# Kernel tuning notes

Measured on AMD Instinct MI355X. Metric: run time of the kernel, lower is better.

Reference implementation:

```python
import jax, jax.numpy as jnp
import numpy as np
import math

N_HEADS = 12
HEAD_SIZE = 64
D_MODEL = 768
N_BASIS = 256
LENGTH = 1024
BATCH = 8
INV_SQRT_2PI = 1.0 / math.sqrt(2.0 * math.pi)


def _phi(t):
    # standard normal pdf
    return INV_SQRT_2PI * jnp.exp(-0.5 * t * t)


def _make_basis():
    # get_gaussian_basis_functions: meshgrid(linspace(0,1,N/2), sigmas).flatten()
    sigmas = np.array([0.01, 0.05], dtype=np.float32)
    mus = np.linspace(0.0, 1.0, N_BASIS // 2, dtype=np.float32)
    mu_b = np.repeat(mus, 2)          # [N]
    sigma_b = np.tile(sigmas, N_BASIS // 2)  # [N]
    return jnp.asarray(mu_b), jnp.asarray(sigma_b)


def _make_G(mu_b, sigma_b, klen, ridge=1.0):
    # compute_G: positions (i+1)/l, F[j,i] = psi_j(pos_i), G = F^T (F F^T + I)^{-1}
    pos = jnp.arange(1, klen + 1, dtype=jnp.float32) / klen
    F = _phi((pos[None, :] - mu_b[:, None]) / sigma_b[:, None]) / sigma_b[:, None]  # [N, klen]
    A = F @ F.T + ridge * jnp.eye(N_BASIS, dtype=jnp.float32)
    return F.T @ jnp.linalg.inv(A)  # [klen, N]


def setup_inputs() -> dict:
    key = jax.random.key(0)
    ks = jax.random.split(key, 8)
    sc = 1.0 / math.sqrt(D_MODEL)
    x = jax.random.normal(ks[0], (LENGTH, BATCH, D_MODEL), jnp.float32)
    q = jax.random.normal(ks[1], (LENGTH, BATCH, D_MODEL), jnp.float32)
    Wq = jax.random.normal(ks[2], (D_MODEL, D_MODEL), jnp.float32) * sc
    Wk = jax.random.normal(ks[3], (D_MODEL, D_MODEL), jnp.float32) * sc
    Wv = jax.random.normal(ks[4], (D_MODEL, D_MODEL), jnp.float32) * sc
    Wo = jax.random.normal(ks[5], (D_MODEL, D_MODEL), jnp.float32) * sc
    w_mu = jax.random.normal(ks[6], (N_BASIS,), jnp.float32) * (1.0 / math.sqrt(N_BASIS))
    w_sigma = jax.random.normal(ks[7], (N_BASIS,), jnp.float32) * (1.0 / math.sqrt(N_BASIS))
    mu_b, sigma_b = _make_basis()
    G = _make_G(mu_b, sigma_b, LENGTH)
    return {"x": x, "q": q, "Wq": Wq, "Wk": Wk, "Wv": Wv, "Wo": Wo,
            "w_mu": w_mu, "w_sigma": w_sigma, "mu_b": mu_b, "sigma_b": sigma_b, "G": G}


def reference(x, q, Wq, Wk, Wv, Wo, w_mu, w_sigma, mu_b, sigma_b, G):
    klen, B, d = x.shape
    qlen = q.shape[0]
    H, dh = N_HEADS, HEAD_SIZE
    # value_function: compress memory onto basis coefficients, B_mat: [B, N, d]
    Bmat = jnp.einsum('lbd,ln->bnd', x, G)
    keys = (Bmat @ Wk.T).reshape(B, N_BASIS, H, dh).transpose(0, 2, 1, 3)    # [B,H,N,dh]
    values = (Bmat @ Wv.T).reshape(B, N_BASIS, H, dh).transpose(0, 2, 1, 3)  # [B,H,N,dh]
    query = (q.transpose(1, 0, 2) @ Wq.T).reshape(B, qlen, H, dh).transpose(0, 2, 1, 3)
    scores = jnp.einsum('bhqe,bhne->bhqn', query, keys) / math.sqrt(dh)      # [B,H,q,N]
    # attention distribution parameters (theta -> (mu, sigma_sq) exactly)
    mu = jax.nn.sigmoid(scores @ w_mu)          # [B,H,q]
    sigma_sq = jax.nn.softplus(scores @ w_sigma)  # [B,H,q]
    # ContinuousSoftmax forward: E_{N(mu,sigma_sq)}[psi_j]
    #   = N(mu; mu_b_j, sigma_b_j^2 + sigma_sq)   (product-of-Gaussians integral)
    s = jnp.sqrt(sigma_b[None, None, None, :] ** 2 + sigma_sq[..., None])
    r = _phi((mu[..., None] - mu_b[None, None, None, :]) / s) / s            # [B,H,q,N]
    context = jnp.einsum('bhqn,bhnd->bhqd', r, values)                       # [B,H,q,dh]
    context = context.transpose(0, 2, 1, 3).reshape(B, qlen, H * dh)
    return context @ Wo.T  # [B, qlen, d_model]
```

## Files before the change

### kernel.cpp

```cpp
#include <hip/hip_runtime.h>
#include <hip/hip_bf16.h>
#include <math.h>

#define NHEADS 12
#define HEAD   64
#define DM     768
#define NB     256
#define SLEN   1024
#define NBATCH 8

typedef __bf16 bf16x8 __attribute__((ext_vector_type(8)));
typedef float  f32x4  __attribute__((ext_vector_type(4)));

__device__ __forceinline__ float gload(const void* p, long i, int bf) {
  return bf ? __bfloat162float(((const __hip_bfloat16*)p)[i])
            : ((const float*)p)[i];
}

__global__ void detect_dtype(const void* x, int* flag) {
  __shared__ float red[256];
  int t = threadIdx.x;
  const __hip_bfloat16* p = (const __hip_bfloat16*)x;
  float a = fabsf(__bfloat162float(p[t * 2]));
  float b = fabsf(__bfloat162float(p[t * 2 + 1]));
  float m = fmaxf(a, b);
  red[t] = m;
  __syncthreads();
  for (int s = 128; s > 0; s >>= 1) {
    if (t < s) red[t] = fmaxf(red[t], red[t + s]);
    __syncthreads();
  }
  if (t == 0) flag[0] = (red[0] < 1e4f) ? 1 : 0;
}

__global__ void convertk(const void* __restrict__ src, float* __restrict__ dst,
                         int n, const int* __restrict__ flagp) {
  int bf = flagp[0];
  int i = blockIdx.x * 256 + threadIdx.x;
  if (i < n) dst[i] = gload(src, i, bf);
}

__global__ __launch_bounds__(256) void zerok(float* __restrict__ p, long n) {
  long i = ((long)blockIdx.x * 256 + threadIdx.x) * 4;
  if (i < n) {
    f32x4 z = {0.f, 0.f, 0.f, 0.f};
    *(f32x4*)(p + i) = z;
  }
}

__global__ __launch_bounds__(256) void split4(
    const void* __restrict__ src, __hip_bfloat16* __restrict__ dh,
    __hip_bfloat16* __restrict__ dl, int n, const int* __restrict__ flagp,
    int use_flag) {
  int bf = use_flag ? flagp[0] : 0;
  int i0 = (blockIdx.x * 256 + threadIdx.x) * 4;
  if (i0 >= n) return;
#pragma unroll
  for (int j = 0; j < 4; j++) {
    float f = gload(src, i0 + j, bf);
    __hip_bfloat16 h = __float2bfloat16(f);
    dh[i0 + j] = h;
    dl[i0 + j] = __float2bfloat16(f - __bfloat162float(h));
  }
}

__global__ __launch_bounds__(256) void tsplit(
    const void* __restrict__ src, __hip_bfloat16* __restrict__ dh,
    __hip_bfloat16* __restrict__ dl, int R, int C,
    const int* __restrict__ flagp) {
  int bf = flagp[0];
  __shared__ float t[64][65];
  int r0 = blockIdx.y * 64, c0 = blockIdx.x * 64;
  int cl = threadIdx.x & 63, rl = threadIdx.x >> 6;
#pragma unroll
  for (int i = 0; i < 16; i++) {
    int rr = rl + i * 4;
    t[rr][cl] = gload(src, (long)(r0 + rr) * C + c0 + cl, bf);
  }
  __syncthreads();
#pragma unroll
  for (int i = 0; i < 16; i++) {
    int cc = rl + i * 4;
    float f = t[cl][cc];
    __hip_bfloat16 h = __float2bfloat16(f);
    long o = (long)(c0 + cc) * R + r0 + cl;
    dh[o] = h;
    dl[o] = __float2bfloat16(f - __bfloat162float(h));
  }
}

__global__ __launch_bounds__(256) void vtsplit(
    const float* __restrict__ src, __hip_bfloat16* __restrict__ dh,
    __hip_bfloat16* __restrict__ dl) {
  __shared__ float tle[64][65];
  const int z = blockIdx.y;
  const int r0 = blockIdx.x * 64;
  const float* s = src + (long)z * 16384;
  int cl = threadIdx.x & 63, rl4 = threadIdx.x >> 6;
#pragma unroll
  for (int i = 0; i < 16; i++) {
    int rr = rl4 + i * 4;
    tle[rr][cl] = s[(r0 + rr) * 64 + cl];
  }
  __syncthreads();
#pragma unroll
  for (int i = 0; i < 16; i++) {
    int cc = rl4 + i * 4;
    float f = tle[cl][cc];
    __hip_bfloat16 h = __float2bfloat16(f);
    long o = (long)z * 16384 + (long)cc * 256 + r0 + cl;
    dh[o] = h;
    dl[o] = __float2bfloat16(f - __bfloat162float(h));
  }
}

__device__ __forceinline__ void stage_tile(
    const __hip_bfloat16* __restrict__ src, int ld, __hip_bfloat16* lds, int t) {
  int row = t >> 2;
  int col = (t & 3) * 8;
  int wavebase = (t >> 6) * 1024;
#pragma unroll
  for (int i = 0; i < 2; i++) {
    const __hip_bfloat16* gp = src + (long)(i * 64 + row) * ld + col;
    __builtin_amdgcn_global_load_lds(
        (const __attribute__((address_space(1))) void*)gp,
        (__attribute__((address_space(3))) void*)((char*)lds + i * 4096 + wavebase),
        16, 0, 0);
  }
}

__global__ __launch_bounds__(256) void mfma_nt_lds(
    const __hip_bfloat16* __restrict__ Ah_g, const __hip_bfloat16* __restrict__ Al_g,
    const __hip_bfloat16* __restrict__ Wh_g, const __hip_bfloat16* __restrict__ Wl_g,
    void* __restrict__ Cout, int K, int lda, int ldb, long a_batch, long c_batch,
    int om, int oh, const int* __restrict__ flagp, int use_flag, int pmask_bf,
    int ksplit) {
  int flag = flagp[0];
  int bf = use_flag ? flag : 0;
  __shared__ __hip_bfloat16 As0[4096], As1[4096];
  __shared__ __hip_bfloat16 Bs0[4096], Bs1[4096];

  const int gx = gridDim.x, gy = gridDim.y;
  const int nwg = gx * gy * gridDim.z;
  const int lin = (blockIdx.z * gy + blockIdx.y) * gx + blockIdx.x;
  const int swz = (lin & 7) * (nwg >> 3) + (lin >> 3);
  const int bx = swz % gx;
  const int rem = swz / gx;
  const int by = rem % gy;
  const int bzf = rem / gy;
  const int bz = bzf / ksplit;
  const int kc = bzf - bz * ksplit;
  const int Ks = K / ksplit;
  const int kbeg = kc * Ks, kend = kbeg + Ks;

  const int m0 = by * 128, n0 = bx * 128;
  const int t = threadIdx.x;
  const int lane = t & 63;
  const int r = lane & 15, g = lane >> 4;
  const int wave = t >> 6;
  const int wm = (wave >> 1) * 64, wn = (wave & 1) * 64;

  const __hip_bfloat16* Abh = Ah_g + (long)bz * a_batch;
  const __hip_bfloat16* Abl = Al_g + (long)bz * a_batch;

  f32x4 zero4 = {0.f, 0.f, 0.f, 0.f};
  f32x4 acc[4][4];
#pragma unroll
  for (int fi = 0; fi < 4; fi++)
#pragma unroll
    for (int fj = 0; fj < 4; fj++) acc[fi][fj] = zero4;

  for (int pass = 0; pass < 3; pass++) {
    if (flag && !((pmask_bf >> pass) & 1)) continue;
    const __hip_bfloat16* Arow = ((pass < 2) ? Abh : Abl) + (long)m0 * lda;
    const __hip_bfloat16* Brow = ((pass == 1) ? Wl_g : Wh_g) + (long)n0 * ldb;
    stage_tile(Arow + kbeg, lda, As0, t);
    stage_tile(Brow + kbeg, ldb, Bs0, t);
    __syncthreads();
    int cur = 0;
    for (int k0 = kbeg; k0 < kend; k0 += 32) {
      const __hip_bfloat16* Asc = cur ? As1 : As0;
      const __hip_bfloat16* Bsc = cur ? Bs1 : Bs0;
      bf16x8 af[4], bw[4];
#pragma unroll
      for (int fi = 0; fi < 4; fi++)
        af[fi] = *(const bf16x8*)(Asc + (wm + fi * 16 + r) * 32 + g * 8);
#pragma unroll
      for (int fj = 0; fj < 4; fj++)
        bw[fj] = *(const bf16x8*)(Bsc + (wn + fj * 16 + r) * 32 + g * 8);
      if (k0 + 32 < kend) {
        stage_tile(Arow + k0 + 32, lda, cur ? As0 : As1, t);
        stage_tile(Brow + k0 + 32, ldb, cur ? Bs0 : Bs1, t);
      }
#pragma unroll
      for (int fi = 0; fi < 4; fi++)
#pragma unroll
        for (int fj = 0; fj < 4; fj++)
          acc[fi][fj] = __builtin_amdgcn_mfma_f32_16x16x32_bf16(
              af[fi], bw[fj], acc[fi][fj], 0, 0, 0);
      __syncthreads();
      cur ^= 1;
    }
  }

  if (ksplit > 1) {
    float* Cf = (float*)Cout;
#pragma unroll
    for (int fi = 0; fi < 4; fi++)
#pragma unroll
      for (int fj = 0; fj < 4; fj++)
#pragma unroll
        for (int v = 0; v < 4; v++) {
          int m = m0 + wm + fi * 16 + g * 4 + v;
          int n = n0 + wn + fj * 16 + r;
          long off = (long)bz * c_batch + (long)m * om + (long)(n >> 6) * oh + (n & 63);
          atomicAdd(Cf + off, acc[fi][fj][v]);
        }
  } else {
#pragma unroll
    for (int fi = 0; fi < 4; fi++)
#pragma unroll
      for (int fj = 0; fj < 4; fj++)
#pragma unroll
        for (int v = 0; v < 4; v++) {
          int m = m0 + wm + fi * 16 + g * 4 + v;
          int n = n0 + wn + fj * 16 + r;
          long off = (long)bz * c_batch + (long)m * om + (long)(n >> 6) * oh + (n & 63);
          float val = acc[fi][fj][v];
          if (bf) ((__hip_bfloat16*)Cout)[off] = __float2bfloat16(val);
          else    ((float*)Cout)[off] = val;
        }
  }
}

__global__ __launch_bounds__(256) void bvec(
    const float* __restrict__ Bmat, const float* __restrict__ wmuf,
    const float* __restrict__ wsigf, float* __restrict__ bmu,
    float* __restrict__ bsig) {
  int t = blockIdx.x * 256 + threadIdx.x;
  int w = t / 6144, r = t % 6144;
  const float* wv = w ? wsigf : wmuf;
  float acc = 0.f;
  for (int n = 0; n < NB; n++) acc += wv[n] * Bmat[(long)n * 6144 + r];
  (w ? bsig : bmu)[r] = acc;
}

__global__ __launch_bounds__(256) void kvec(
    const float* __restrict__ Wkf, const float* __restrict__ bmu,
    const float* __restrict__ bsig, float* __restrict__ kmu,
    float* __restrict__ ksig) {
  int t = blockIdx.x * 256 + threadIdx.x;
  int w = t / 6144, r = t % 6144;
  int b = r / 768, c = r % 768;
  const float* bv = (w ? bsig : bmu) + b * 768;
  const float* wk = Wkf + (long)c * 768;
  float acc = 0.f;
  for (int d = 0; d < 768; d++) acc += bv[d] * wk[d];
  (w ? ksig : kmu)[r] = acc;
}

__global__ __launch_bounds__(256) void wqvec(
    const float* __restrict__ Wqf, const float* __restrict__ kmu,
    const float* __restrict__ ksig, float* __restrict__ wqm,
    float* __restrict__ wqs) {
  int t = blockIdx.x * 256 + threadIdx.x;
  int w = t / 73728, r = t % 73728;
  int b = r / 9216, h = (r % 9216) / 768, d = r % 768;
  const float* kv = (w ? ksig : kmu) + b * 768 + h * 64;
  float acc = 0.f;
  for (int dh = 0; dh < 64; dh++)
    acc += Wqf[(long)(h * 64 + dh) * 768 + d] * kv[dh];
  (w ? wqs : wqm)[r] = acc;
}

__global__ __launch_bounds__(256) void amu_kernel(
    const void* __restrict__ q, const float* __restrict__ wqm,
    const float* __restrict__ wqs, float* __restrict__ amu,
    const int* __restrict__ flagp) {
  int bf = flagp[0];
  int lane = threadIdx.x & 63;
  int wave = threadIdx.x >> 6;
  int qrow = blockIdx.x * 4 + wave;
  int b = blockIdx.y;
  float qv[12];
  long base = ((long)qrow * 8 + b) * 768 + lane;
#pragma unroll
  for (int j = 0; j < 12; j++) qv[j] = gload(q, base + 64 * j, bf);
  for (int hh = 0; hh < 24; hh++) {
    const float* vec = (hh < 12) ? (wqm + ((long)b * 12 + hh) * 768)
                                 : (wqs + ((long)b * 12 + hh - 12) * 768);
    float p = 0.f;
#pragma unroll
    for (int j = 0; j < 12; j++) p += qv[j] * vec[lane + 64 * j];
#pragma unroll
    for (int m = 32; m >= 1; m >>= 1) p += __shfl_xor(p, m);
    if (lane == 0) amu[((long)b * 24 + hh) * 1024 + qrow] = p;
  }
}

__global__ __launch_bounds__(256) void attn_mfma(
    const __hip_bfloat16* __restrict__ Vth, const __hip_bfloat16* __restrict__ Vtl,
    const float* __restrict__ amu, const float* __restrict__ mubf,
    const float* __restrict__ sigbf, __hip_bfloat16* __restrict__ Ch,
    __hip_bfloat16* __restrict__ Cl) {
  const int qch = blockIdx.x, h = blockIdx.y, b = blockIdx.z;
  const int t = threadIdx.x;
  const int lane = t & 63, wave = t >> 6;
  const int r = lane & 15, g = lane >> 4;
  const int wq = wave * 32;
  __shared__ float s_mub[NB], s_sb2[NB];
  {
    float sb = sigbf[t];
    s_mub[t] = mubf[t];
    s_sb2[t] = sb * sb;
  }
  __syncthreads();

  float mu_[2], sig_[2];
#pragma unroll
  for (int fi = 0; fi < 2; fi++) {
    int q = qch * 128 + wq + fi * 16 + r;
    float araw = amu[((long)b * 24 + h) * 1024 + q] * 0.125f;
    float sraw = amu[((long)b * 24 + 12 + h) * 1024 + q] * 0.125f;
    mu_[fi] = 1.f / (1.f + expf(-araw));
    sig_[fi] = fmaxf(sraw, 0.f) + log1pf(expf(-fabsf(sraw)));
  }

  const __hip_bfloat16* vhb = Vth + ((long)b * 12 + h) * 16384;
  const __hip_bfloat16* vlb = Vtl + ((long)b * 12 + h) * 16384;

  f32x4 zero4 = {0.f, 0.f, 0.f, 0.f};
  f32x4 acc[2][4];
#pragma unroll
  for (int fi = 0; fi < 2; fi++)
#pragma unroll
    for (int fj = 0; fj < 4; fj++) acc[fi][fj] = zero4;

  for (int ks = 0; ks < 8; ks++) {
    bf16x8 rh[2], rl[2];
#pragma unroll
    for (int fi = 0; fi < 2; fi++) {
      float mu = mu_[fi], sg = sig_[fi];
#pragma unroll
      for (int j = 0; j < 8; j++) {
        int n = ks * 32 + g * 8 + j;
        float inv_s = rsqrtf(s_sb2[n] + sg);
        float tt = (mu - s_mub[n]) * inv_s;
        float rv = 0.3989422804014327f * inv_s *
                   exp2f(-0.7213475204444817f * tt * tt);
        __bf16 hi = (__bf16)rv;
        rh[fi][j] = hi;
        rl[fi][j] = (__bf16)(rv - (float)hi);
      }
    }
#pragma unroll
    for (int fj = 0; fj < 4; fj++) {
      long vo = (long)(fj * 16 + r) * 256 + ks * 32 + g * 8;
      bf16x8 vh = *(const bf16x8*)(vhb + vo);
      bf16x8 vl = *(const bf16x8*)(vlb + vo);
#pragma unroll
      for (int fi = 0; fi < 2; fi++) {
        acc[fi][fj] = __builtin_amdgcn_mfma_f32_16x16x32_bf16(
            rh[fi], vh, acc[fi][fj], 0, 0, 0);
        acc[fi][fj] = __builtin_amdgcn_mfma_f32_16x16x32_bf16(
            rl[fi], vh, acc[fi][fj], 0, 0, 0);
        acc[fi][fj] = __builtin_amdgcn_mfma_f32_16x16x32_bf16(
            rh[fi], vl, acc[fi][fj], 0, 0, 0);
      }
    }
  }

#pragma unroll
  for (int fi = 0; fi < 2; fi++)
#pragma unroll
    for (int fj = 0; fj < 4; fj++)
#pragma unroll
      for (int v = 0; v < 4; v++) {
        int q = qch * 128 + wq + fi * 16 + g * 4 + v;
        int d = fj * 16 + r;
        long off = ((long)(b * SLEN + q)) * DM + h * HEAD + d;
        float f = acc[fi][fj][v];
        __hip_bfloat16 hh = __float2bfloat16(f);
        Ch[off] = hh;
        Cl[off] = __float2bfloat16(f - __bfloat162float(hh));
      }
}

extern "C" void kernel_launch(void* const* d_in, const int* in_sizes, int n_in,
                              void* d_out, int out_size, void* d_ws, size_t ws_size,
                              hipStream_t stream) {
  const void* x    = d_in[0];
  const void* q    = d_in[1];
  const void* Wq   = d_in[2];
  const void* Wk   = d_in[3];
  const void* Wv   = d_in[4];
  const void* Wo   = d_in[5];
  const void* wmu  = d_in[6];
  const void* wsig = d_in[7];
  const void* mub  = d_in[8];
  const void* sigb = d_in[9];
  const void* G    = d_in[10];

  int* flagp = (int*)d_ws;
  float* base = (float*)d_ws + 16;
  float* Wqf   = base;
  float* Wkf   = Wqf + 589824;
  float* wmuf  = Wkf + 589824;
  float* wsigf = wmuf + 256;
  float* mubf  = wsigf + 256;
  float* sigbf = mubf + 256;
  float* Bmat  = sigbf + 256;
  float* values= Bmat + 1572864;
  float* bmu   = values + 1572864;
  float* bsig  = bmu + 6144;
  float* kmu   = bsig + 6144;
  float* ksig  = kmu + 6144;
  float* wqm   = ksig + 6144;
  float* wqs   = wqm + 73728;
  float* amu   = wqs + 73728;
  __hip_bfloat16* Wvh = (__hip_bfloat16*)(amu + 196608);
  __hip_bfloat16* Wvl = Wvh + 589824;
  __hip_bfloat16* Woh = Wvl + 589824;
  __hip_bfloat16* Wol = Woh + 589824;
  __hip_bfloat16* Gth = Wol + 589824;
  __hip_bfloat16* Gtl = Gth + 262144;
  __hip_bfloat16* Bh  = Gtl + 262144;
  __hip_bfloat16* Bl  = Bh + 1572864;
  __hip_bfloat16* XCh = Bl + 1572864;
  __hip_bfloat16* XCl = XCh + 6291456;
  __hip_bfloat16* Vth = XCl + 6291456;
  __hip_bfloat16* Vtl = Vth + 1572864;

  detect_dtype<<<1, 256, 0, stream>>>(x, flagp);

  convertk<<<2304, 256, 0, stream>>>(Wq, Wqf, 589824, flagp);
  convertk<<<2304, 256, 0, stream>>>(Wk, Wkf, 589824, flagp);
  convertk<<<1, 256, 0, stream>>>(wmu, wmuf, 256, flagp);
  convertk<<<1, 256, 0, stream>>>(wsig, wsigf, 256, flagp);
  convertk<<<1, 256, 0, stream>>>(mub, mubf, 256, flagp);
  convertk<<<1, 256, 0, stream>>>(sigb, sigbf, 256, flagp);

  tsplit<<<dim3(4, 16), 256, 0, stream>>>(G, Gth, Gtl, 1024, 256, flagp);
  tsplit<<<dim3(96, 16), 256, 0, stream>>>(x, XCh, XCl, 1024, 6144, flagp);
  split4<<<576, 256, 0, stream>>>(Wv, Wvh, Wvl, 589824, flagp, 1);
  split4<<<576, 256, 0, stream>>>(Wo, Woh, Wol, 589824, flagp, 1);

  zerok<<<1536, 256, 0, stream>>>(Bmat, 1572864);
  mfma_nt_lds<<<dim3(48, 2, 8), 256, 0, stream>>>(
      Gth, Gtl, XCh, XCl, Bmat, 1024, 1024, 1024,
      0, 0, 6144, 64, flagp, 0,
      1, 8);

  split4<<<1536, 256, 0, stream>>>(Bmat, Bh, Bl, 1572864, flagp, 0);

  zerok<<<1536, 256, 0, stream>>>(values, 1572864);
  mfma_nt_lds<<<dim3(6, 2, 64), 256, 0, stream>>>(
      Bh, Bl, Wvh, Wvl, values, 768, 6144, 768,
      768, 196608, 64, 16384, flagp, 0,
      5, 8);

  vtsplit<<<dim3(4, 96), 256, 0, stream>>>(values, Vth, Vtl);

  bvec<<<48, 256, 0, stream>>>(Bmat, wmuf, wsigf, bmu, bsig);
  kvec<<<48, 256, 0, stream>>>(Wkf, bmu, bsig, kmu, ksig);
  wqvec<<<576, 256, 0, stream>>>(Wqf, kmu, ksig, wqm, wqs);
  amu_kernel<<<dim3(256, 8), 256, 0, stream>>>(q, wqm, wqs, amu, flagp);

  attn_mfma<<<dim3(8, 12, 8), 256, 0, stream>>>(
      Vth, Vtl, amu, mubf, sigbf, XCh, XCl);

  mfma_nt_lds<<<dim3(6, 64, 1), 256, 0, stream>>>(
      XCh, XCl, Woh, Wol, d_out, 768, 768, 768,
      0, 0, 768, 64, flagp, 1,
      5, 1);
}
```

Baseline: 423.1 us.

## Fuse prep launches, replace atomic split-K with slabs, fuse vector chain

Merges the separate convert, transpose-split and split kernels into one multi-role prep launch, cutting the number of launches. The split-K GEMMs now use 4 splits instead of 8 and write partial results to separate slabs instead of using atomicAdd into zeroed buffers. Follow-up kernels sum the slabs and fuse that sum with the bf16 hi/lo split, so the zeroing kernels go away. The bvec, kvec and wqvec kernels are fused into a single 16-block chain kernel. The trade-offs are that this chain kernel has far less parallelism, that the slabs take more memory traffic, and that one slab buffer is aliased onto the XC buffer.

```diff
diff --git a/kernel.cpp b/kernel.cpp
--- a/kernel.cpp
+++ b/kernel.cpp
@@ -33,84 +33,79 @@
   if (t == 0) flag[0] = (red[0] < 1e4f) ? 1 : 0;
 }
 
-__global__ void convertk(const void* __restrict__ src, float* __restrict__ dst,
-                         int n, const int* __restrict__ flagp) {
-  int bf = flagp[0];
-  int i = blockIdx.x * 256 + threadIdx.x;
-  if (i < n) dst[i] = gload(src, i, bf);
-}
-
-__global__ __launch_bounds__(256) void zerok(float* __restrict__ p, long n) {
-  long i = ((long)blockIdx.x * 256 + threadIdx.x) * 4;
-  if (i < n) {
-    f32x4 z = {0.f, 0.f, 0.f, 0.f};
-    *(f32x4*)(p + i) = z;
-  }
-}
-
-__global__ __launch_bounds__(256) void split4(
-    const void* __restrict__ src, __hip_bfloat16* __restrict__ dh,
-    __hip_bfloat16* __restrict__ dl, int n, const int* __restrict__ flagp,
-    int use_flag) {
-  int bf = use_flag ? flagp[0] : 0;
-  int i0 = (blockIdx.x * 256 + threadIdx.x) * 4;
-  if (i0 >= n) return;
-#pragma unroll
-  for (int j = 0; j < 4; j++) {
-    float f = gload(src, i0 + j, bf);
-    __hip_bfloat16 h = __float2bfloat16(f);
-    dh[i0 + j] = h;
-    dl[i0 + j] = __float2bfloat16(f - __bfloat162float(h));
-  }
-}
-
-__global__ __launch_bounds__(256) void tsplit(
-    const void* __restrict__ src, __hip_bfloat16* __restrict__ dh,
-    __hip_bfloat16* __restrict__ dl, int R, int C,
+__global__ __launch_bounds__(256) void prep(
+    const void* __restrict__ Wq, const void* __restrict__ Wk,
+    const void* __restrict__ wmu, const void* __restrict__ wsig,
+    const void* __restrict__ mub, const void* __restrict__ sigb,
+    const void* __restrict__ G, const void* __restrict__ x,
+    const void* __restrict__ Wv, const void* __restrict__ Wo,
+    float* __restrict__ Wqf, float* __restrict__ Wkf,
+    float* __restrict__ wmuf, float* __restrict__ wsigf,
+    float* __restrict__ mubf, float* __restrict__ sigbf,
+    __hip_bfloat16* __restrict__ Gth, __hip_bfloat16* __restrict__ Gtl,
+    __hip_bfloat16* __restrict__ XCh, __hip_bfloat16* __restrict__ XCl,
+    __hip_bfloat16* __restrict__ Wvh, __hip_bfloat16* __restrict__ Wvl,
+    __hip_bfloat16* __restrict__ Woh, __hip_bfloat16* __restrict__ Wol,
     const int* __restrict__ flagp) {
-  int bf = flagp[0];
-  __shared__ float t[64][65];
-  int r0 = blockIdx.y * 64, c0 = blockIdx.x * 64;
-  int cl = threadIdx.x & 63, rl = threadIdx.x >> 6;
-#pragma unroll
-  for (int i = 0; i < 16; i++) {
-    int rr = rl + i * 4;
-    t[rr][cl] = gload(src, (long)(r0 + rr) * C + c0 + cl, bf);
-  }
-  __syncthreads();
-#pragma unroll
-  for (int i = 0; i < 16; i++) {
-    int cc = rl + i * 4;
-    float f = t[cl][cc];
-    __hip_bfloat16 h = __float2bfloat16(f);
-    long o = (long)(c0 + cc) * R + r0 + cl;
-    dh[o] = h;
-    dl[o] = __float2bfloat16(f - __bfloat162float(h));
-  }
-}
-
-__global__ __launch_bounds__(256) void vtsplit(
-    const float* __restrict__ src, __hip_bfloat16* __restrict__ dh,
-    __hip_bfloat16* __restrict__ dl) {
-  __shared__ float tle[64][65];
-  const int z = blockIdx.y;
-  const int r0 = blockIdx.x * 64;
-  const float* s = src + (long)z * 16384;
-  int cl = threadIdx.x & 63, rl4 = threadIdx.x >> 6;
-#pragma unroll
-  for (int i = 0; i < 16; i++) {
-    int rr = rl4 + i * 4;
-    tle[rr][cl] = s[(r0 + rr) * 64 + cl];
-  }
-  __syncthreads();
-#pragma unroll
-  for (int i = 0; i < 16; i++) {
-    int cc = rl4 + i * 4;
-    float f = tle[cl][cc];
-    __hip_bfloat16 h = __float2bfloat16(f);
-    long o = (long)z * 16384 + (long)cc * 256 + r0 + cl;
-    dh[o] = h;
-    dl[o] = __float2bfloat16(f - __bfloat162float(h));
+  __shared__ float tl[64][65];
+  const int blk = blockIdx.x, tid = threadIdx.x;
+  const int bf = flagp[0];
+
+  if (blk < 1152) {
+    const void* src = (blk < 576) ? Wq : Wk;
+    float* dst = (blk < 576) ? Wqf : Wkf;
+    int rb = (blk < 576) ? blk : blk - 576;
+    int i0 = (rb * 256 + tid) * 4;
+#pragma unroll
+    for (int j = 0; j < 4; j++) dst[i0 + j] = gload(src, i0 + j, bf);
+  } else if (blk < 1156) {
+    int which = blk - 1152;
+    const void* src = (which == 0) ? wmu : (which == 1) ? wsig
+                      : (which == 2) ? mub : sigb;
+    float* dst = (which == 0) ? wmuf : (which == 1) ? wsigf
+                 : (which == 2) ? mubf : sigbf;
+    dst[tid] = gload(src, tid, bf);
+  } else if (blk < 2756) {
+    const void* src;
+    __hip_bfloat16 *dh, *dl;
+    int R = 1024, C, bx, by;
+    if (blk < 1220) {
+      int sub = blk - 1156;
+      src = G; dh = Gth; dl = Gtl; C = 256; bx = sub % 4; by = sub / 4;
+    } else {
+      int sub = blk - 1220;
+      src = x; dh = XCh; dl = XCl; C = 6144; bx = sub % 96; by = sub / 96;
+    }
+    int r0 = by * 64, c0 = bx * 64;
+    int cl = tid & 63, rl = tid >> 6;
+#pragma unroll
+    for (int i = 0; i < 16; i++) {
+      int rr = rl + i * 4;
+      tl[rr][cl] = gload(src, (long)(r0 + rr) * C + c0 + cl, bf);
+    }
+    __syncthreads();
+#pragma unroll
+    for (int i = 0; i < 16; i++) {
+      int cc = rl + i * 4;
+      float f = tl[cl][cc];
+      __hip_bfloat16 h = __float2bfloat16(f);
+      long o = (long)(c0 + cc) * R + r0 + cl;
+      dh[o] = h;
+      dl[o] = __float2bfloat16(f - __bfloat162float(h));
+    }
+  } else {
+    const void* src = (blk < 3332) ? Wv : Wo;
+    __hip_bfloat16* dh = (blk < 3332) ? Wvh : Woh;
+    __hip_bfloat16* dl = (blk < 3332) ? Wvl : Wol;
+    int rb = (blk < 3332) ? blk - 2756 : blk - 3332;
+    int i0 = (rb * 256 + tid) * 4;
+#pragma unroll
+    for (int j = 0; j < 4; j++) {
+      float f = gload(src, i0 + j, bf);
+      __hip_bfloat16 h = __float2bfloat16(f);
+      dh[i0 + j] = h;
+      dl[i0 + j] = __float2bfloat16(f - __bfloat162float(h));
+    }
   }
 }
 
@@ -134,7 +129,7 @@
     const __hip_bfloat16* __restrict__ Wh_g, const __hip_bfloat16* __restrict__ Wl_g,
     void* __restrict__ Cout, int K, int lda, int ldb, long a_batch, long c_batch,
     int om, int oh, const int* __restrict__ flagp, int use_flag, int pmask_bf,
-    int ksplit) {
+    int ksplit, long kslab) {
   int flag = flagp[0];
   int bf = use_flag ? flag : 0;
   __shared__ __hip_bfloat16 As0[4096], As1[4096];
@@ -204,7 +199,7 @@
   }
 
   if (ksplit > 1) {
-    float* Cf = (float*)Cout;
+    float* Cf = (float*)Cout + (long)kc * kslab;
 #pragma unroll
     for (int fi = 0; fi < 4; fi++)
 #pragma unroll
@@ -214,7 +209,7 @@
           int m = m0 + wm + fi * 16 + g * 4 + v;
           int n = n0 + wn + fj * 16 + r;
           long off = (long)bz * c_batch + (long)m * om + (long)(n >> 6) * oh + (n & 63);
-          atomicAdd(Cf + off, acc[fi][fj][v]);
+          Cf[off] = acc[fi][fj][v];
         }
   } else {
 #pragma unroll
@@ -233,44 +228,89 @@
   }
 }
 
-__global__ __launch_bounds__(256) void bvec(
+__global__ __launch_bounds__(256) void reduce_split(
+    const float* __restrict__ slabs, float* __restrict__ outf,
+    __hip_bfloat16* __restrict__ dh, __hip_bfloat16* __restrict__ dl) {
+  long i0 = ((long)blockIdx.x * 256 + threadIdx.x) * 4;
+  f32x4 s = *(const f32x4*)(slabs + i0);
+#pragma unroll
+  for (int k = 1; k < 4; k++) {
+    f32x4 v = *(const f32x4*)(slabs + (long)k * 1572864 + i0);
+    s.x += v.x; s.y += v.y; s.z += v.z; s.w += v.w;
+  }
+  *(f32x4*)(outf + i0) = s;
+#pragma unroll
+  for (int j = 0; j < 4; j++) {
+    float f = s[j];
+    __hip_bfloat16 h = __float2bfloat16(f);
+    dh[i0 + j] = h;
+    dl[i0 + j] = __float2bfloat16(f - __bfloat162float(h));
+  }
+}
+
+__global__ __launch_bounds__(256) void vtsplit_sum(
+    const float* __restrict__ slabs, __hip_bfloat16* __restrict__ dh,
+    __hip_bfloat16* __restrict__ dl) {
+  __shared__ float tle[64][65];
+  const int z = blockIdx.y;
+  const int r0 = blockIdx.x * 64;
+  int cl = threadIdx.x & 63, rl4 = threadIdx.x >> 6;
+#pragma unroll
+  for (int i = 0; i < 16; i++) {
+    int rr = rl4 + i * 4;
+    long idx = (long)z * 16384 + (r0 + rr) * 64 + cl;
+    float s = slabs[idx];
+#pragma unroll
+    for (int k = 1; k < 4; k++) s += slabs[(long)k * 1572864 + idx];
+    tle[rr][cl] = s;
+  }
+  __syncthreads();
+#pragma unroll
+  for (int i = 0; i < 16; i++) {
+    int cc = rl4 + i * 4;
+    float f = tle[cl][cc];
+    __hip_bfloat16 h = __float2bfloat16(f);
+    long o = (long)z * 16384 + (long)cc * 256 + r0 + cl;
+    dh[o] = h;
+    dl[o] = __float2bfloat16(f - __bfloat162float(h));
+  }
+}
+
+__global__ __launch_bounds__(256) void chain(
     const float* __restrict__ Bmat, const float* __restrict__ wmuf,
-    const float* __restrict__ wsigf, float* __restrict__ bmu,
-    float* __restrict__ bsig) {
-  int t = blockIdx.x * 256 + threadIdx.x;
-  int w = t / 6144, r = t % 6144;
+    const float* __restrict__ wsigf, const float* __restrict__ Wkf,
+    const float* __restrict__ Wqf, float* __restrict__ wqm,
+    float* __restrict__ wqs) {
+  const int b = blockIdx.x >> 1, w = blockIdx.x & 1;
+  const int tid = threadIdx.x;
+  __shared__ float bv[768], kv[768];
   const float* wv = w ? wsigf : wmuf;
-  float acc = 0.f;
-  for (int n = 0; n < NB; n++) acc += wv[n] * Bmat[(long)n * 6144 + r];
-  (w ? bsig : bmu)[r] = acc;
-}
-
-__global__ __launch_bounds__(256) void kvec(
-    const float* __restrict__ Wkf, const float* __restrict__ bmu,
-    const float* __restrict__ bsig, float* __restrict__ kmu,
-    float* __restrict__ ksig) {
-  int t = blockIdx.x * 256 + threadIdx.x;
-  int w = t / 6144, r = t % 6144;
-  int b = r / 768, c = r % 768;
-  const float* bv = (w ? bsig : bmu) + b * 768;
-  const float* wk = Wkf + (long)c * 768;
-  float acc = 0.f;
-  for (int d = 0; d < 768; d++) acc += bv[d] * wk[d];
-  (w ? ksig : kmu)[r] = acc;
-}
-
-__global__ __launch_bounds__(256) void wqvec(
-    const float* __restrict__ Wqf, const float* __restrict__ kmu,
-    const float* __restrict__ ksig, float* __restrict__ wqm,
-    float* __restrict__ wqs) {
-  int t = blockIdx.x * 256 + threadIdx.x;
-  int w = t / 73728, r = t % 73728;
-  int b = r / 9216, h = (r % 9216) / 768, d = r % 768;
-  const float* kv = (w ? ksig : kmu) + b * 768 + h * 64;
-  float acc = 0.f;
-  for (int dh = 0; dh < 64; dh++)
-    acc += Wqf[(long)(h * 64 + dh) * 768 + d] * kv[dh];
-  (w ? wqs : wqm)[r] = acc;
+#pragma unroll
+  for (int u = 0; u < 3; u++) {
+    int d = tid + u * 256;
+    float a = 0.f;
+    for (int n = 0; n < NB; n++) a += wv[n] * Bmat[(long)n * 6144 + b * 768 + d];
+    bv[d] = a;
+  }
+  __syncthreads();
+#pragma unroll
+  for (int u = 0; u < 3; u++) {
+    int c = tid + u * 256;
+    float a = 0.f;
+    for (int d = 0; d < 768; d++) a += bv[d] * Wkf[(long)c * 768 + d];
+    kv[c] = a;
+  }
+  __syncthreads();
+  float* outp = (w ? wqs : wqm) + (long)b * 9216;
+  for (int u = 0; u < 36; u++) {
+    int j = tid + u * 256;
+    int h = j / 768, d = j % 768;
+    float a = 0.f;
+#pragma unroll
+    for (int dh = 0; dh < 64; dh++)
+      a += Wqf[(long)(h * 64 + dh) * 768 + d] * kv[h * 64 + dh];
+    outp[j] = a;
+  }
 }
 
 __global__ __launch_bounds__(256) void amu_kernel(
@@ -410,12 +450,8 @@
   float* mubf  = wsigf + 256;
   float* sigbf = mubf + 256;
   float* Bmat  = sigbf + 256;
-  float* values= Bmat + 1572864;
-  float* bmu   = values + 1572864;
-  float* bsig  = bmu + 6144;
-  float* kmu   = bsig + 6144;
-  float* ksig  = kmu + 6144;
-  float* wqm   = ksig + 6144;
+  float* slab1 = Bmat + 1572864;
+  float* wqm   = slab1 + 6291456;
   float* wqs   = wqm + 73728;
   float* amu   = wqs + 73728;
   __hip_bfloat16* Wvh = (__hip_bfloat16*)(amu + 196608);
@@ -428,42 +464,32 @@
   __hip_bfloat16* Bl  = Bh + 1572864;
   __hip_bfloat16* XCh = Bl + 1572864;
   __hip_bfloat16* XCl = XCh + 6291456;
+  float* slab2 = (float*)XCh;
   __hip_bfloat16* Vth = XCl + 6291456;
   __hip_bfloat16* Vtl = Vth + 1572864;
 
   detect_dtype<<<1, 256, 0, stream>>>(x, flagp);
 
-  convertk<<<2304, 256, 0, stream>>>(Wq, Wqf, 589824, flagp);
-  convertk<<<2304, 256, 0, stream>>>(Wk, Wkf, 589824, flagp);
-  convertk<<<1, 256, 0, stream>>>(wmu, wmuf, 256, flagp);
-  convertk<<<1, 256, 0, stream>>>(wsig, wsigf, 256, flagp);
-  convertk<<<1, 256, 0, stream>>>(mub, mubf, 256, flagp);
-  convertk<<<1, 256, 0, stream>>>(sigb, sigbf, 256, flagp);
-
-  tsplit<<<dim3(4, 16), 256, 0, stream>>>(G, Gth, Gtl, 1024, 256, flagp);
-  tsplit<<<dim3(96, 16), 256, 0, stream>>>(x, XCh, XCl, 1024, 6144, flagp);
-  split4<<<576, 256, 0, stream>>>(Wv, Wvh, Wvl, 589824, flagp, 1);
-  split4<<<576, 256, 0, stream>>>(Wo, Woh, Wol, 589824, flagp, 1);
-
-  zerok<<<1536, 256, 0, stream>>>(Bmat, 1572864);
-  mfma_nt_lds<<<dim3(48, 2, 8), 256, 0, stream>>>(
-      Gth, Gtl, XCh, XCl, Bmat, 1024, 1024, 1024,
+  prep<<<3908, 256, 0, stream>>>(
+      Wq, Wk, wmu, wsig, mub, sigb, G, x, Wv, Wo,
+      Wqf, Wkf, wmuf, wsigf, mubf, sigbf,
+      Gth, Gtl, XCh, XCl, Wvh, Wvl, Woh, Wol, flagp);
+
+  mfma_nt_lds<<<dim3(48, 2, 4), 256, 0, stream>>>(
+      Gth, Gtl, XCh, XCl, slab1, 1024, 1024, 1024,
       0, 0, 6144, 64, flagp, 0,
-      1, 8);
-
-  split4<<<1536, 256, 0, stream>>>(Bmat, Bh, Bl, 1572864, flagp, 0);
-
-  zerok<<<1536, 256, 0, stream>>>(values, 1572864);
-  mfma_nt_lds<<<dim3(6, 2, 64), 256, 0, stream>>>(
-      Bh, Bl, Wvh, Wvl, values, 768, 6144, 768,
+      1, 4, 1572864);
+
+  reduce_split<<<1536, 256, 0, stream>>>(slab1, Bmat, Bh, Bl);
+
+  mfma_nt_lds<<<dim3(6, 2, 32), 256, 0, stream>>>(
+      Bh, Bl, Wvh, Wvl, slab2, 768, 6144, 768,
       768, 196608, 64, 16384, flagp, 0,
-      5, 8);
-
-  vtsplit<<<dim3(4, 96), 256, 0, stream>>>(values, Vth, Vtl);
-
-  bvec<<<48, 256, 0, stream>>>(Bmat, wmuf, wsigf, bmu, bsig);
-  kvec<<<48, 256, 0, stream>>>(Wkf, bmu, bsig, kmu, ksig);
-  wqvec<<<576, 256, 0, stream>>>(Wqf, kmu, ksig, wqm, wqs);
+      5, 4, 1572864);
+
+  vtsplit_sum<<<dim3(4, 96), 256, 0, stream>>>(slab2, Vth, Vtl);
+
+  chain<<<16, 256, 0, stream>>>(Bmat, wmuf, wsigf, Wkf, Wqf, wqm, wqs);
   amu_kernel<<<dim3(256, 8), 256, 0, stream>>>(q, wqm, wqs, amu, flagp);
 
   attn_mfma<<<dim3(8, 12, 8), 256, 0, stream>>>(
@@ -472,5 +498,5 @@
   mfma_nt_lds<<<dim3(6, 64, 1), 256, 0, stream>>>(
       XCh, XCl, Woh, Wol, d_out, 768, 768, 768,
       0, 0, 768, 64, flagp, 1,
-      5, 1);
-}
+      5, 1, 0);
+}
```

New measurement: 661.8 us. 56.4% more time.
